# Performance work log

Measured on AMD Instinct MI355X. Metric: run time of the kernel, lower is better.

The kernel has to match this reference:

```python
import jax, jax.numpy as jnp
import numpy as np

WIN = 16  # win_size == stride


def setup_inputs() -> dict:
    key = jax.random.key(0)
    k0, k1, k2 = jax.random.split(key, 3)
    B, M, D, H = 32, 2048, 512, 64  # H = input_size // time_ratio
    return {
        "x": jax.random.normal(k0, (B, M, D), dtype=jnp.float32),
        "W1": jax.random.normal(k1, (D, H), dtype=jnp.float32) / np.sqrt(D).astype(np.float32),
        "b1": jnp.zeros((H,), jnp.float32),
        "W2": jax.random.normal(k2, (H, D), dtype=jnp.float32) / np.sqrt(H).astype(np.float32),
        "b2": jnp.zeros((D,), jnp.float32),
    }


def _softsign(v):
    return v / (1.0 + jnp.abs(v))


def reference(x, W1, b1, W2, b2):
    B, M, D = x.shape
    pad_total = (-M) % WIN
    lo = pad_total // 2
    hi = pad_total - lo
    xp = jnp.pad(x, ((0, 0), (lo, hi), (0, 0)), mode="edge")
    Mp = M + pad_total
    nW = Mp // WIN
    xw = xp.reshape(B, nW, WIN, D)
    m = xw.mean(axis=2)                     # windowed mean-pool -> [B, nW, D]
    h = _softsign(jnp.einsum("bwd,dh->bwh", m, W1) + b1)
    g = jax.nn.sigmoid(_softsign(jnp.einsum("bwh,hd->bwd", h, W2) + b2))  # [B, nW, D]
    y = (xw * g[:, :, None, :]).reshape(B, Mp, D)  # broadcast gate over window
    return y[:, lo:lo + M, :]
```

## Files before the change

kernel.cpp:

```cpp
#include <hip/hip_runtime.h>
#include <cmath>


constexpr int WIN = 16;
constexpr int D   = 512;
constexpr int H   = 64;
constexpr int TPB = 256;
constexpr int NW  = 2;

__global__ __launch_bounds__(TPB, 4) void se_block_kernel(
    const float* __restrict__ x,
    const float* __restrict__ W1,
    const float* __restrict__ b1,
    const float* __restrict__ W2,
    const float* __restrict__ b2,
    float* __restrict__ y)
{
    const int tid = threadIdx.x;
    const size_t base = (size_t)blockIdx.x * (size_t)(NW * WIN * D);
    const float4* __restrict__ xw = reinterpret_cast<const float4*>(x + base);
    float4*       __restrict__ yw = reinterpret_cast<float4*>(y + base);

    const float4* __restrict__ W1f4 = reinterpret_cast<const float4*>(W1);
    const float4* __restrict__ W2f4 = reinterpret_cast<const float4*>(W2);
    const float4* __restrict__ b2f4 = reinterpret_cast<const float4*>(b2);

    __shared__ float4 s_ps[NW][TPB];
    __shared__ float4 s_m4[NW][D / 4];
    __shared__ float4 s_hp[16][NW][H / 4];
    __shared__ float  s_h[NW][H];
    __shared__ float4 s_gp[2][NW][D / 4];
    __shared__ float4 s_g4[NW][D / 4];

    float4 r[NW][8];
#pragma unroll
    for (int w = 0; w < NW; ++w)
#pragma unroll
        for (int i = 0; i < 8; ++i) r[w][i] = xw[w * 2048 + i * TPB + tid];

#pragma unroll
    for (int w = 0; w < NW; ++w) {
        float4 ps = r[w][0];
#pragma unroll
        for (int i = 1; i < 8; ++i) {
            ps.x += r[w][i].x; ps.y += r[w][i].y; ps.z += r[w][i].z; ps.w += r[w][i].w;
        }
        s_ps[w][tid] = ps;
    }
    __syncthreads();
    {
        const int w = tid >> 7;
        const int c = tid & 127;
        const float4 a = s_ps[w][c];
        const float4 b = s_ps[w][c + 128];
        const float sc = 1.0f / 16.0f;
        float4 m;
        m.x = (a.x + b.x) * sc; m.y = (a.y + b.y) * sc;
        m.z = (a.z + b.z) * sc; m.w = (a.w + b.w) * sc;
        s_m4[w][c] = m;
    }
    __syncthreads();

    {
        const int p  = tid >> 4;
        const int j4 = tid & 15;
        float4 acc[NW];
#pragma unroll
        for (int w = 0; w < NW; ++w) acc[w] = make_float4(0.f, 0.f, 0.f, 0.f);
#pragma unroll 2
        for (int kk4 = 0; kk4 < 8; ++kk4) {
            const int c4 = p * 8 + kk4;
            const int k  = c4 * 4;
            const float4 w0 = W1f4[(size_t)(k + 0) * 16 + j4];
            const float4 w1 = W1f4[(size_t)(k + 1) * 16 + j4];
            const float4 w2 = W1f4[(size_t)(k + 2) * 16 + j4];
            const float4 w3 = W1f4[(size_t)(k + 3) * 16 + j4];
#pragma unroll
            for (int w = 0; w < NW; ++w) {
                const float4 mv = s_m4[w][c4];
                acc[w].x = fmaf(mv.x, w0.x, acc[w].x); acc[w].y = fmaf(mv.x, w0.y, acc[w].y);
                acc[w].z = fmaf(mv.x, w0.z, acc[w].z); acc[w].w = fmaf(mv.x, w0.w, acc[w].w);
                acc[w].x = fmaf(mv.y, w1.x, acc[w].x); acc[w].y = fmaf(mv.y, w1.y, acc[w].y);
                acc[w].z = fmaf(mv.y, w1.z, acc[w].z); acc[w].w = fmaf(mv.y, w1.w, acc[w].w);
                acc[w].x = fmaf(mv.z, w2.x, acc[w].x); acc[w].y = fmaf(mv.z, w2.y, acc[w].y);
                acc[w].z = fmaf(mv.z, w2.z, acc[w].z); acc[w].w = fmaf(mv.z, w2.w, acc[w].w);
                acc[w].x = fmaf(mv.w, w3.x, acc[w].x); acc[w].y = fmaf(mv.w, w3.y, acc[w].y);
                acc[w].z = fmaf(mv.w, w3.z, acc[w].z); acc[w].w = fmaf(mv.w, w3.w, acc[w].w);
            }
        }
#pragma unroll
        for (int w = 0; w < NW; ++w) s_hp[p][w][j4] = acc[w];
    }
    __syncthreads();

    if (tid < NW * H) {
        const float* s_hpf = reinterpret_cast<const float*>(s_hp);
        const int w = tid >> 6;
        const int j = tid & 63;
        float s = b1[j];
#pragma unroll
        for (int p = 0; p < 16; ++p) s += s_hpf[(p * NW + w) * H + j];
        s_h[w][j] = s / (1.0f + fabsf(s));
    }
    __syncthreads();

    {
        const float4* s_h4 = reinterpret_cast<const float4*>(&s_h[0][0]);
        const int q  = tid >> 7;
        const int d4 = tid & 127;
        float4 acc[NW];
#pragma unroll
        for (int w = 0; w < NW; ++w) acc[w] = make_float4(0.f, 0.f, 0.f, 0.f);
#pragma unroll 2
        for (int jj4 = 0; jj4 < 8; ++jj4) {
            const int jg = q * 8 + jj4;
            const int j  = jg * 4;
            const float4 w0 = W2f4[(size_t)(j + 0) * 128 + d4];
            const float4 w1 = W2f4[(size_t)(j + 1) * 128 + d4];
            const float4 w2 = W2f4[(size_t)(j + 2) * 128 + d4];
            const float4 w3 = W2f4[(size_t)(j + 3) * 128 + d4];
#pragma unroll
            for (int w = 0; w < NW; ++w) {
                const float4 hv = s_h4[w * 16 + jg];
                acc[w].x = fmaf(hv.x, w0.x, acc[w].x); acc[w].y = fmaf(hv.x, w0.y, acc[w].y);
                acc[w].z = fmaf(hv.x, w0.z, acc[w].z); acc[w].w = fmaf(hv.x, w0.w, acc[w].w);
                acc[w].x = fmaf(hv.y, w1.x, acc[w].x); acc[w].y = fmaf(hv.y, w1.y, acc[w].y);
                acc[w].z = fmaf(hv.y, w1.z, acc[w].z); acc[w].w = fmaf(hv.y, w1.w, acc[w].w);
                acc[w].x = fmaf(hv.z, w2.x, acc[w].x); acc[w].y = fmaf(hv.z, w2.y, acc[w].y);
                acc[w].z = fmaf(hv.z, w2.z, acc[w].z); acc[w].w = fmaf(hv.z, w2.w, acc[w].w);
                acc[w].x = fmaf(hv.w, w3.x, acc[w].x); acc[w].y = fmaf(hv.w, w3.y, acc[w].y);
                acc[w].z = fmaf(hv.w, w3.z, acc[w].z); acc[w].w = fmaf(hv.w, w3.w, acc[w].w);
            }
        }
#pragma unroll
        for (int w = 0; w < NW; ++w) s_gp[q][w][d4] = acc[w];
    }
    __syncthreads();

    {
        const int w  = tid >> 7;
        const int d4 = tid & 127;
        const float4 a  = s_gp[0][w][d4];
        const float4 b  = s_gp[1][w][d4];
        const float4 bb = b2f4[d4];
        float4 s;
        s.x = a.x + b.x + bb.x; s.y = a.y + b.y + bb.y;
        s.z = a.z + b.z + bb.z; s.w = a.w + b.w + bb.w;
        s.x = s.x / (1.0f + fabsf(s.x)); s.y = s.y / (1.0f + fabsf(s.y));
        s.z = s.z / (1.0f + fabsf(s.z)); s.w = s.w / (1.0f + fabsf(s.w));
        float4 g;
        g.x = 1.0f / (1.0f + __expf(-s.x)); g.y = 1.0f / (1.0f + __expf(-s.y));
        g.z = 1.0f / (1.0f + __expf(-s.z)); g.w = 1.0f / (1.0f + __expf(-s.w));
        s_g4[w][d4] = g;
    }
    __syncthreads();

    {
        const int c = tid & 127;
#pragma unroll
        for (int w = 0; w < NW; ++w) {
            const float4 g = s_g4[w][c];
#pragma unroll
            for (int i = 0; i < 8; ++i) {
                float4 o;
                o.x = r[w][i].x * g.x; o.y = r[w][i].y * g.y;
                o.z = r[w][i].z * g.z; o.w = r[w][i].w * g.w;
                yw[w * 2048 + i * TPB + tid] = o;
            }
        }
    }
}

extern "C" void kernel_launch(void* const* d_in, const int* in_sizes, int n_in,
                              void* d_out, int out_size, void* d_ws, size_t ws_size,
                              hipStream_t stream) {
    const float* x  = (const float*)d_in[0];
    const float* W1 = (const float*)d_in[1];
    const float* b1 = (const float*)d_in[2];
    const float* W2 = (const float*)d_in[3];
    const float* b2 = (const float*)d_in[4];
    float* y = (float*)d_out;

    const int n_windows = in_sizes[0] / (WIN * D);
    const int n_blocks  = n_windows / NW;
    se_block_kernel<<<dim3(n_blocks), dim3(TPB), 0, stream>>>(x, W1, b1, W2, b2, y);
}
```

Baseline: 56.43 us.

## Drop register-held window data, reload x for gating, alias shared buffers

The kernel no longer keeps all 16 float4 values of x in registers between the mean pass and the gating pass. It re-reads x from global memory (hopefully from L2/MALL) when writing the output. Shared memory buffers are aliased into two regions, the separate mean stage is folded into the first GEMV, and the launch_bounds occupancy hint is removed. The aim is lower register and LDS pressure so more blocks can be resident. The cost is a second read of x, which can add HBM traffic if the cache misses, plus extra barriers.

```diff
diff --git a/kernel.cpp b/kernel.cpp
--- a/kernel.cpp
+++ b/kernel.cpp
@@ -8,7 +8,7 @@
 constexpr int TPB = 256;
 constexpr int NW  = 2;
 
-__global__ __launch_bounds__(TPB, 4) void se_block_kernel(
+__global__ __launch_bounds__(TPB) void se_block_kernel(
     const float* __restrict__ x,
     const float* __restrict__ W1,
     const float* __restrict__ b1,
@@ -25,39 +25,24 @@
     const float4* __restrict__ W2f4 = reinterpret_cast<const float4*>(W2);
     const float4* __restrict__ b2f4 = reinterpret_cast<const float4*>(b2);
 
-    __shared__ float4 s_ps[NW][TPB];
-    __shared__ float4 s_m4[NW][D / 4];
-    __shared__ float4 s_hp[16][NW][H / 4];
-    __shared__ float  s_h[NW][H];
-    __shared__ float4 s_gp[2][NW][D / 4];
-    __shared__ float4 s_g4[NW][D / 4];
+    __shared__ __align__(16) char s_regionA[NW * TPB * 16];
+    __shared__ __align__(16) char s_regionB[16 * NW * 16 * 16];
+    __shared__ float s_h[NW][H];
 
-    float4 r[NW][8];
-#pragma unroll
-    for (int w = 0; w < NW; ++w)
-#pragma unroll
-        for (int i = 0; i < 8; ++i) r[w][i] = xw[w * 2048 + i * TPB + tid];
+    float4* s_ps = reinterpret_cast<float4*>(s_regionA);
+    float4* s_gp = reinterpret_cast<float4*>(s_regionA);
+    float4* s_hp = reinterpret_cast<float4*>(s_regionB);
+    float4* s_g4 = reinterpret_cast<float4*>(s_regionB);
 
 #pragma unroll
     for (int w = 0; w < NW; ++w) {
-        float4 ps = r[w][0];
+        float4 ps = make_float4(0.f, 0.f, 0.f, 0.f);
 #pragma unroll
-        for (int i = 1; i < 8; ++i) {
-            ps.x += r[w][i].x; ps.y += r[w][i].y; ps.z += r[w][i].z; ps.w += r[w][i].w;
+        for (int i = 0; i < 8; ++i) {
+            const float4 v = xw[w * 2048 + i * TPB + tid];
+            ps.x += v.x; ps.y += v.y; ps.z += v.z; ps.w += v.w;
         }
-        s_ps[w][tid] = ps;
-    }
-    __syncthreads();
-    {
-        const int w = tid >> 7;
-        const int c = tid & 127;
-        const float4 a = s_ps[w][c];
-        const float4 b = s_ps[w][c + 128];
-        const float sc = 1.0f / 16.0f;
-        float4 m;
-        m.x = (a.x + b.x) * sc; m.y = (a.y + b.y) * sc;
-        m.z = (a.z + b.z) * sc; m.w = (a.w + b.w) * sc;
-        s_m4[w][c] = m;
+        s_ps[w * TPB + tid] = ps;
     }
     __syncthreads();
 
@@ -77,19 +62,28 @@
             const float4 w3 = W1f4[(size_t)(k + 3) * 16 + j4];
 #pragma unroll
             for (int w = 0; w < NW; ++w) {
-                const float4 mv = s_m4[w][c4];
-                acc[w].x = fmaf(mv.x, w0.x, acc[w].x); acc[w].y = fmaf(mv.x, w0.y, acc[w].y);
-                acc[w].z = fmaf(mv.x, w0.z, acc[w].z); acc[w].w = fmaf(mv.x, w0.w, acc[w].w);
-                acc[w].x = fmaf(mv.y, w1.x, acc[w].x); acc[w].y = fmaf(mv.y, w1.y, acc[w].y);
-                acc[w].z = fmaf(mv.y, w1.z, acc[w].z); acc[w].w = fmaf(mv.y, w1.w, acc[w].w);
-                acc[w].x = fmaf(mv.z, w2.x, acc[w].x); acc[w].y = fmaf(mv.z, w2.y, acc[w].y);
-                acc[w].z = fmaf(mv.z, w2.z, acc[w].z); acc[w].w = fmaf(mv.z, w2.w, acc[w].w);
-                acc[w].x = fmaf(mv.w, w3.x, acc[w].x); acc[w].y = fmaf(mv.w, w3.y, acc[w].y);
-                acc[w].z = fmaf(mv.w, w3.z, acc[w].z); acc[w].w = fmaf(mv.w, w3.w, acc[w].w);
+                const float4 a = s_ps[w * TPB + c4];
+                const float4 b = s_ps[w * TPB + c4 + 128];
+                const float mv0 = a.x + b.x, mv1 = a.y + b.y;
+                const float mv2 = a.z + b.z, mv3 = a.w + b.w;
+                acc[w].x = fmaf(mv0, w0.x, acc[w].x); acc[w].y = fmaf(mv0, w0.y, acc[w].y);
+                acc[w].z = fmaf(mv0, w0.z, acc[w].z); acc[w].w = fmaf(mv0, w0.w, acc[w].w);
+                acc[w].x = fmaf(mv1, w1.x, acc[w].x); acc[w].y = fmaf(mv1, w1.y, acc[w].y);
+                acc[w].z = fmaf(mv1, w1.z, acc[w].z); acc[w].w = fmaf(mv1, w1.w, acc[w].w);
+                acc[w].x = fmaf(mv2, w2.x, acc[w].x); acc[w].y = fmaf(mv2, w2.y, acc[w].y);
+                acc[w].z = fmaf(mv2, w2.z, acc[w].z); acc[w].w = fmaf(mv2, w2.w, acc[w].w);
+                acc[w].x = fmaf(mv3, w3.x, acc[w].x); acc[w].y = fmaf(mv3, w3.y, acc[w].y);
+                acc[w].z = fmaf(mv3, w3.z, acc[w].z); acc[w].w = fmaf(mv3, w3.w, acc[w].w);
             }
         }
+        __syncthreads();
+        const float sc = 1.0f / 16.0f;
 #pragma unroll
-        for (int w = 0; w < NW; ++w) s_hp[p][w][j4] = acc[w];
+        for (int w = 0; w < NW; ++w) {
+            float4 v = acc[w];
+            v.x *= sc; v.y *= sc; v.z *= sc; v.w *= sc;
+            s_hp[(p * NW + w) * 16 + j4] = v;
+        }
     }
     __syncthreads();
 
@@ -132,16 +126,17 @@
                 acc[w].z = fmaf(hv.w, w3.z, acc[w].z); acc[w].w = fmaf(hv.w, w3.w, acc[w].w);
             }
         }
+        __syncthreads();
 #pragma unroll
-        for (int w = 0; w < NW; ++w) s_gp[q][w][d4] = acc[w];
+        for (int w = 0; w < NW; ++w) s_gp[(q * NW + w) * 128 + d4] = acc[w];
     }
     __syncthreads();
 
     {
         const int w  = tid >> 7;
         const int d4 = tid & 127;
-        const float4 a  = s_gp[0][w][d4];
-        const float4 b  = s_gp[1][w][d4];
+        const float4 a  = s_gp[(0 * NW + w) * 128 + d4];
+        const float4 b  = s_gp[(1 * NW + w) * 128 + d4];
         const float4 bb = b2f4[d4];
         float4 s;
         s.x = a.x + b.x + bb.x; s.y = a.y + b.y + bb.y;
@@ -151,7 +146,8 @@
         float4 g;
         g.x = 1.0f / (1.0f + __expf(-s.x)); g.y = 1.0f / (1.0f + __expf(-s.y));
         g.z = 1.0f / (1.0f + __expf(-s.z)); g.w = 1.0f / (1.0f + __expf(-s.w));
-        s_g4[w][d4] = g;
+        __syncthreads();
+        s_g4[w * 128 + d4] = g;
     }
     __syncthreads();
 
@@ -159,12 +155,12 @@
         const int c = tid & 127;
 #pragma unroll
         for (int w = 0; w < NW; ++w) {
-            const float4 g = s_g4[w][c];
+            const float4 g = s_g4[w * 128 + c];
 #pragma unroll
             for (int i = 0; i < 8; ++i) {
+                const float4 v = xw[w * 2048 + i * TPB + tid];
                 float4 o;
-                o.x = r[w][i].x * g.x; o.y = r[w][i].y * g.y;
-                o.z = r[w][i].z * g.z; o.w = r[w][i].w * g.w;
+                o.x = v.x * g.x; o.y = v.y * g.y; o.z = v.z * g.z; o.w = v.w * g.w;
                 yw[w * 2048 + i * TPB + tid] = o;
             }
         }
```

Measured after the change: 65.63 us. 1.16x slower.
